# Optimization experiments

Hardware: AMD Instinct MI355X
Metric: run time of the kernel (lower is better)

## Reference

```python
import jax, jax.numpy as jnp
import numpy as np

N_NODES = 100000
N_EDGES = 3200000
D = 128


def setup_inputs() -> dict:
    key = jax.random.key(0)
    k1, k2, k3 = jax.random.split(key, 3)
    x = jax.random.normal(k1, (N_NODES, D), dtype=jnp.float32)
    edge_index = jax.random.randint(k2, (2, N_EDGES), 0, N_NODES, dtype=jnp.int64)
    W = jax.random.normal(k3, (D, D), dtype=jnp.float32) / np.sqrt(D)
    b = jnp.zeros((D,), dtype=jnp.float32)
    return {"x": x, "edge_index": edge_index, "W": W, "b": b}


def reference(x, edge_index, W, b):
    N = x.shape[0]
    # GCNConv: add self loops
    loop = jnp.arange(N, dtype=edge_index.dtype)
    src = jnp.concatenate([edge_index[0], loop])  # message source j
    dst = jnp.concatenate([edge_index[1], loop])  # aggregation target i
    # symmetric normalization: deg counted at targets (incl. self loops)
    deg = jax.ops.segment_sum(jnp.ones_like(dst, dtype=x.dtype), dst, num_segments=N)
    dinv = deg ** -0.5  # every node has deg >= 1 due to self loops
    norm = dinv[src] * dinv[dst]  # [E+N]
    # linear transform then gather-scale-scatter aggregation
    h = x @ W  # [N, D_out]
    msgs = h[src] * norm[:, None]  # [E+N, D_out]
    out = jax.ops.segment_sum(msgs, dst, num_segments=N) + b
    return jax.nn.relu(out)
```

## Files before the change

kernel.cpp:

```cpp
#include <hip/hip_runtime.h>

#define NN 100000
#define NE 3200000
#define DD 128
#define NB 391
#define NCH 256
#define CHUNK (NE / NCH)
#define PSTAGE 9216


typedef __attribute__((ext_vector_type(8))) short bf16x8;
typedef __attribute__((ext_vector_type(4))) float f32x4;

__device__ inline unsigned bf16pair(float a, float b) {
    unsigned ua = __float_as_uint(a); ua = (ua + 0x7fffu + ((ua >> 16) & 1u)) >> 16;
    unsigned ub = __float_as_uint(b); ub = (ub + 0x7fffu + ((ub >> 16) & 1u)) >> 16;
    return ua | (ub << 16);
}
__device__ inline float bflo(unsigned u) { return __uint_as_float(u << 16); }
__device__ inline float bfhi(unsigned u) { return __uint_as_float(u & 0xffff0000u); }

__global__ __launch_bounds__(256) void k_hist1(const int* __restrict__ dst, int* __restrict__ H,
                                               const float* __restrict__ W, unsigned* __restrict__ Wimg) {
    if (blockIdx.x < 32) {
        int i = blockIdx.x * 256 + threadIdx.x;
        int c = i >> 6, k2 = i & 63;
        unsigned v = bf16pair(W[(size_t)(k2 * 2) * DD + c], W[(size_t)(k2 * 2 + 1) * DD + c]);
        int byte = c * 256 + ((k2 * 4) ^ ((c & 7) << 4));
        *(unsigned*)((char*)Wimg + byte) = v;
    }
    __shared__ int h[NB];
    for (int i = threadIdx.x; i < NB; i += 256) h[i] = 0;
    __syncthreads();
    const int base = blockIdx.x * CHUNK;
    for (int i = threadIdx.x; i < CHUNK; i += 256)
        atomicAdd(&h[dst[base + i] >> 8], 1);
    __syncthreads();
    for (int i = threadIdx.x; i < NB; i += 256) H[blockIdx.x * NB + i] = h[i];
}

__global__ __launch_bounds__(256) void k_offB1(int* __restrict__ H, int* __restrict__ BT) {
    __shared__ int s[256];
    const int b = blockIdx.x;
    const int t = threadIdx.x;
    int v = H[t * NB + b];
    s[t] = v;
    __syncthreads();
    for (int off = 1; off < 256; off <<= 1) {
        int u = (t >= off) ? s[t - off] : 0;
        __syncthreads();
        s[t] += u;
        __syncthreads();
    }
    H[t * NB + b] = s[t] - v;
    if (t == 255) BT[b] = s[255];
}

__global__ __launch_bounds__(512) void k_offB2(const int* __restrict__ BT, int* __restrict__ BB) {
    __shared__ int s[512];
    const int t = threadIdx.x;
    int v = (t < NB) ? BT[t] : 0;
    s[t] = v;
    __syncthreads();
    for (int off = 1; off < 512; off <<= 1) {
        int u = (t >= off) ? s[t - off] : 0;
        __syncthreads();
        s[t] += u;
        __syncthreads();
    }
    if (t < NB) BB[t] = s[t] - v;
}

__global__ __launch_bounds__(256) void k_part(const int* __restrict__ src, const int* __restrict__ dst,
                                              const int* __restrict__ H, const int* __restrict__ BB,
                                              unsigned* __restrict__ P) {
    __shared__ int cur[NB];
    for (int i = threadIdx.x; i < NB; i += 256)
        cur[i] = BB[i] + H[blockIdx.x * NB + i];
    __syncthreads();
    const int base = blockIdx.x * CHUNK;
    for (int i = threadIdx.x; i < CHUNK; i += 256) {
        int s = src[base + i];
        int d = dst[base + i];
        int p = atomicAdd(&cur[d >> 8], 1);
        P[p] = ((unsigned)s << 8) | (unsigned)(d & 255);
    }
}

__global__ __launch_bounds__(256) void k_bsort(const unsigned* __restrict__ P, const int* __restrict__ BB,
                                               const int* __restrict__ BT, int* __restrict__ esrc,
                                               int* __restrict__ cnt, int* __restrict__ start) {
    __shared__ int hist[256], red[256], sexcl[256], fil[256];
    __shared__ unsigned Ps[PSTAGE];
    const int b = blockIdx.x;
    const int base = BB[b];
    const int n = BT[b];
    const int t = threadIdx.x;
    const bool fits = (n <= PSTAGE);
    hist[t] = 0;
    __syncthreads();
    for (int i = t; i < n; i += 256) {
        unsigned p = P[base + i];
        if (fits) Ps[i] = p;
        atomicAdd(&hist[p & 255u], 1);
    }
    __syncthreads();
    int c = hist[t];
    red[t] = c;
    __syncthreads();
    for (int off = 1; off < 256; off <<= 1) {
        int u = (t >= off) ? red[t - off] : 0;
        __syncthreads();
        red[t] += u;
        __syncthreads();
    }
    int excl = red[t] - c;
    sexcl[t] = excl;
    fil[t] = 0;
    int node = (b << 8) + t;
    if (node < NN) { cnt[node] = c; start[node] = base + excl; }
    __syncthreads();
    for (int i = t; i < n; i += 256) {
        unsigned p = fits ? Ps[i] : P[base + i];
        int dl = (int)(p & 255u);
        int pos = atomicAdd(&fil[dl], 1);
        esrc[base + sexcl[dl] + pos] = (int)(p >> 8);
    }
}

__global__ __launch_bounds__(256) void k_gemm_mfma(
    const float* __restrict__ x, const unsigned* __restrict__ Wimg,
    const int* __restrict__ cnt, unsigned* __restrict__ g) {
    __shared__ unsigned Wl[8192];
    const int tid = threadIdx.x;
    {
        const uint4* s4 = (const uint4*)Wimg;
        uint4* d4 = (uint4*)Wl;
        for (int i = tid; i < 2048; i += 256) d4[i] = s4[i];
    }
    const int row0 = blockIdx.x * 128;
    const int w = tid >> 6;
    const int l = tid & 63;
    const int lr = l & 15, lk = l >> 4;
    bf16x8 a[2][4];
#pragma unroll
    for (int rg = 0; rg < 2; ++rg) {
        int r = row0 + w * 32 + rg * 16 + lr;
        if (r > NN - 1) r = NN - 1;
        const float* xr = x + (size_t)r * DD;
#pragma unroll
        for (int kk = 0; kk < 4; ++kk) {
            float4 f0 = *(const float4*)(xr + kk * 32 + lk * 8);
            float4 f1 = *(const float4*)(xr + kk * 32 + lk * 8 + 4);
            uint4 wv;
            wv.x = bf16pair(f0.x, f0.y); wv.y = bf16pair(f0.z, f0.w);
            wv.z = bf16pair(f1.x, f1.y); wv.w = bf16pair(f1.z, f1.w);
            a[rg][kk] = *(bf16x8*)&wv;
        }
    }
    __syncthreads();
    f32x4 acc[2][8];
#pragma unroll
    for (int rg = 0; rg < 2; ++rg)
#pragma unroll
        for (int t = 0; t < 8; ++t) acc[rg][t] = (f32x4){0.f, 0.f, 0.f, 0.f};
#pragma unroll
    for (int t = 0; t < 8; ++t) {
        int c = t * 16 + lr;
#pragma unroll
        for (int kk = 0; kk < 4; ++kk) {
            int byte = c * 256 + ((kk * 64 + lk * 16) ^ ((c & 7) << 4));
            bf16x8 bfr = *(bf16x8*)((char*)Wl + byte);
            acc[0][t] = __builtin_amdgcn_mfma_f32_16x16x32_bf16(a[0][kk], bfr, acc[0][t], 0, 0, 0);
            acc[1][t] = __builtin_amdgcn_mfma_f32_16x16x32_bf16(a[1][kk], bfr, acc[1][t], 0, 0, 0);
        }
    }
#pragma unroll
    for (int rg = 0; rg < 2; ++rg)
#pragma unroll
    for (int j = 0; j < 4; ++j) {
        int row = row0 + w * 32 + rg * 16 + lk * 4 + j;
        if (row < NN) {
            float dinv = rsqrtf((float)(cnt[row] + 1));
#pragma unroll
            for (int t = 0; t < 4; ++t) {
                unsigned v = bf16pair(acc[rg][t][j] * dinv, acc[rg][t + 4][j] * dinv);
                g[(size_t)row * 64 + t * 16 + lr] = v;
            }
        }
    }
}

__global__ __launch_bounds__(256) void k_aggregate(
    const unsigned* __restrict__ g, const int* __restrict__ esrc,
    const int* __restrict__ start, const int* __restrict__ cnt,
    const float* __restrict__ b, float* __restrict__ out) {
    int node = blockIdx.x * 4 + (threadIdx.x >> 6);
    if (node >= NN) return;
    int lane = threadIdx.x & 63;
    unsigned u0 = g[(unsigned)node * 64u + lane];
    float ax = bflo(u0), ay = bfhi(u0);
    const int base = start[node];
    const int n = cnt[node];
    const int* ep = esrc + base;
    int j = 0;
    for (; j + 16 <= n; j += 16) {
        unsigned v[16];
#pragma unroll
        for (int u = 0; u < 16; ++u)
            v[u] = g[(unsigned)ep[j + u] * 64u + lane];
#pragma unroll
        for (int u = 0; u < 16; ++u) { ax += bflo(v[u]); ay += bfhi(v[u]); }
    }
    for (; j + 4 <= n; j += 4) {
        unsigned v0 = g[(unsigned)ep[j + 0] * 64u + lane];
        unsigned v1 = g[(unsigned)ep[j + 1] * 64u + lane];
        unsigned v2 = g[(unsigned)ep[j + 2] * 64u + lane];
        unsigned v3 = g[(unsigned)ep[j + 3] * 64u + lane];
        ax += bflo(v0) + bflo(v1) + bflo(v2) + bflo(v3);
        ay += bfhi(v0) + bfhi(v1) + bfhi(v2) + bfhi(v3);
    }
    for (; j < n; ++j) {
        unsigned v = g[(unsigned)ep[j] * 64u + lane];
        ax += bflo(v); ay += bfhi(v);
    }
    float dinv = rsqrtf((float)(n + 1));
    float bx = b[lane], by = b[lane + 64];
    float ox = fmaxf(fmaf(ax, dinv, bx), 0.f);
    float oy = fmaxf(fmaf(ay, dinv, by), 0.f);
    __builtin_nontemporal_store(ox, &out[(size_t)node * DD + lane]);
    __builtin_nontemporal_store(oy, &out[(size_t)node * DD + lane + 64]);
}

extern "C" void kernel_launch(void* const* d_in, const int* in_sizes, int n_in,
                              void* d_out, int out_size, void* d_ws, size_t ws_size,
                              hipStream_t stream) {
    const float* x = (const float*)d_in[0];
    const int* edge = (const int*)d_in[1];
    const float* W = (const float*)d_in[2];
    const float* b = (const float*)d_in[3];
    float* out = (float*)d_out;

    char* ws = (char*)d_ws;
    int* cnt      = (int*)(ws);
    int* start    = (int*)(ws + 400 * 1024);
    int* BT       = (int*)(ws + 800 * 1024);
    int* BB       = (int*)(ws + 804 * 1024);
    unsigned* Wim = (unsigned*)(ws + 832 * 1024);
    int* H        = (int*)(ws + (1 << 20));
    int* esrc     = (int*)(ws + (2 << 20));
    unsigned* P   = (unsigned*)(ws + (15ull << 20));
    unsigned* g   = (unsigned*)(ws + (15ull << 20));

    const int* src = edge;
    const int* dst = edge + NE;

    k_hist1<<<NCH, 256, 0, stream>>>(dst, H, W, Wim);
    k_offB1<<<NB, 256, 0, stream>>>(H, BT);
    k_offB2<<<1, 512, 0, stream>>>(BT, BB);
    k_part<<<NCH, 256, 0, stream>>>(src, dst, H, BB, P);
    k_bsort<<<NB, 256, 0, stream>>>(P, BB, BT, esrc, cnt, start);
    k_gemm_mfma<<<(NN + 127) / 128, 256, 0, stream>>>(x, Wim, cnt, g);
    k_aggregate<<<(NN + 3) / 4, 256, 0, stream>>>(g, esrc, start, cnt, b, out);
}
```

Before: 201.2 us.

## Slice gathered features into column slabs and drop the global bucket-offset scan kernel

The intermediate feature matrix is stored as 8 column slices of 32 bytes per node, so each aggregation block handles one slice and a wave gathers 8 neighbours at once. The aim is a smaller L2 working set per slice pass and better cache locality for random gathers. A partial-sum shuffle reduction combines the 8 slots. Separately, the single-block offB2 scan is replaced by an atomicAdd on a global cursor, which saves one launch. That makes bucket order nondeterministic, but each bucket's range stays contiguous. The catch is that each gather now moves only 32-byte segments and edge indices are reread 8 times.

```diff
diff --git a/kernel.cpp b/kernel.cpp
--- a/kernel.cpp
+++ b/kernel.cpp
@@ -7,6 +7,7 @@
 #define NCH 256
 #define CHUNK (NE / NCH)
 #define PSTAGE 9216
+#define SL (NN * 8)
 
 
 typedef __attribute__((ext_vector_type(8))) short bf16x8;
@@ -21,7 +22,9 @@
 __device__ inline float bfhi(unsigned u) { return __uint_as_float(u & 0xffff0000u); }
 
 __global__ __launch_bounds__(256) void k_hist1(const int* __restrict__ dst, int* __restrict__ H,
-                                               const float* __restrict__ W, unsigned* __restrict__ Wimg) {
+                                               const float* __restrict__ W, unsigned* __restrict__ Wimg,
+                                               int* __restrict__ gcur) {
+    if (blockIdx.x == 0 && threadIdx.x == 0) *gcur = 0;
     if (blockIdx.x < 32) {
         int i = blockIdx.x * 256 + threadIdx.x;
         int c = i >> 6, k2 = i & 63;
@@ -39,7 +42,8 @@
     for (int i = threadIdx.x; i < NB; i += 256) H[blockIdx.x * NB + i] = h[i];
 }
 
-__global__ __launch_bounds__(256) void k_offB1(int* __restrict__ H, int* __restrict__ BT) {
+__global__ __launch_bounds__(256) void k_offB1(int* __restrict__ H, int* __restrict__ BT,
+                                               int* __restrict__ BB, int* __restrict__ gcur) {
     __shared__ int s[256];
     const int b = blockIdx.x;
     const int t = threadIdx.x;
@@ -53,22 +57,10 @@
         __syncthreads();
     }
     H[t * NB + b] = s[t] - v;
-    if (t == 255) BT[b] = s[255];
-}
-
-__global__ __launch_bounds__(512) void k_offB2(const int* __restrict__ BT, int* __restrict__ BB) {
-    __shared__ int s[512];
-    const int t = threadIdx.x;
-    int v = (t < NB) ? BT[t] : 0;
-    s[t] = v;
-    __syncthreads();
-    for (int off = 1; off < 512; off <<= 1) {
-        int u = (t >= off) ? s[t - off] : 0;
-        __syncthreads();
-        s[t] += u;
-        __syncthreads();
-    }
-    if (t < NB) BB[t] = s[t] - v;
+    if (t == 255) {
+        BT[b] = s[255];
+        BB[b] = atomicAdd(gcur, s[255]);
+    }
 }
 
 __global__ __launch_bounds__(256) void k_part(const int* __restrict__ src, const int* __restrict__ dst,
@@ -130,7 +122,7 @@
 
 __global__ __launch_bounds__(256) void k_gemm_mfma(
     const float* __restrict__ x, const unsigned* __restrict__ Wimg,
-    const int* __restrict__ cnt, unsigned* __restrict__ g) {
+    const int* __restrict__ cnt, unsigned* __restrict__ g_s) {
     __shared__ unsigned Wl[8192];
     const int tid = threadIdx.x;
     {
@@ -184,52 +176,60 @@
             float dinv = rsqrtf((float)(cnt[row] + 1));
 #pragma unroll
             for (int t = 0; t < 4; ++t) {
+                int col = t * 16 + lr;
                 unsigned v = bf16pair(acc[rg][t][j] * dinv, acc[rg][t + 4][j] * dinv);
-                g[(size_t)row * 64 + t * 16 + lr] = v;
+                g_s[(size_t)(col >> 3) * SL + (size_t)row * 8 + (col & 7)] = v;
             }
         }
     }
 }
 
 __global__ __launch_bounds__(256) void k_aggregate(
-    const unsigned* __restrict__ g, const int* __restrict__ esrc,
+    const unsigned* __restrict__ g_s, const int* __restrict__ esrc,
     const int* __restrict__ start, const int* __restrict__ cnt,
     const float* __restrict__ b, float* __restrict__ out) {
-    int node = blockIdx.x * 4 + (threadIdx.x >> 6);
-    if (node >= NN) return;
-    int lane = threadIdx.x & 63;
-    unsigned u0 = g[(unsigned)node * 64u + lane];
-    float ax = bflo(u0), ay = bfhi(u0);
+    const int slice = blockIdx.x & 7;
+    const int node = (blockIdx.x >> 3) * 4 + (threadIdx.x >> 6);
+    const int lane = threadIdx.x & 63;
+    const int slot = lane >> 3;
+    const int c = lane & 7;
+    const unsigned* gs = g_s + (size_t)slice * SL + c;
+    float ax = 0.f, ay = 0.f;
+    if (slot == 0) {
+        unsigned v = gs[(unsigned)node * 8u];
+        ax = bflo(v); ay = bfhi(v);
+    }
     const int base = start[node];
     const int n = cnt[node];
     const int* ep = esrc + base;
     int j = 0;
-    for (; j + 16 <= n; j += 16) {
-        unsigned v[16];
-#pragma unroll
-        for (int u = 0; u < 16; ++u)
-            v[u] = g[(unsigned)ep[j + u] * 64u + lane];
-#pragma unroll
-        for (int u = 0; u < 16; ++u) { ax += bflo(v[u]); ay += bfhi(v[u]); }
-    }
-    for (; j + 4 <= n; j += 4) {
-        unsigned v0 = g[(unsigned)ep[j + 0] * 64u + lane];
-        unsigned v1 = g[(unsigned)ep[j + 1] * 64u + lane];
-        unsigned v2 = g[(unsigned)ep[j + 2] * 64u + lane];
-        unsigned v3 = g[(unsigned)ep[j + 3] * 64u + lane];
+    for (; j + 32 <= n; j += 32) {
+        unsigned v0 = gs[(unsigned)ep[j + slot] * 8u];
+        unsigned v1 = gs[(unsigned)ep[j + 8 + slot] * 8u];
+        unsigned v2 = gs[(unsigned)ep[j + 16 + slot] * 8u];
+        unsigned v3 = gs[(unsigned)ep[j + 24 + slot] * 8u];
         ax += bflo(v0) + bflo(v1) + bflo(v2) + bflo(v3);
         ay += bfhi(v0) + bfhi(v1) + bfhi(v2) + bfhi(v3);
     }
-    for (; j < n; ++j) {
-        unsigned v = g[(unsigned)ep[j] * 64u + lane];
+    for (; j + 8 <= n; j += 8) {
+        unsigned v = gs[(unsigned)ep[j + slot] * 8u];
         ax += bflo(v); ay += bfhi(v);
     }
-    float dinv = rsqrtf((float)(n + 1));
-    float bx = b[lane], by = b[lane + 64];
-    float ox = fmaxf(fmaf(ax, dinv, bx), 0.f);
-    float oy = fmaxf(fmaf(ay, dinv, by), 0.f);
-    __builtin_nontemporal_store(ox, &out[(size_t)node * DD + lane]);
-    __builtin_nontemporal_store(oy, &out[(size_t)node * DD + lane + 64]);
+    if (j < n && slot < n - j) {
+        unsigned v = gs[(unsigned)ep[j + slot] * 8u];
+        ax += bflo(v); ay += bfhi(v);
+    }
+    ax += __shfl_xor(ax, 8);  ay += __shfl_xor(ay, 8);
+    ax += __shfl_xor(ax, 16); ay += __shfl_xor(ay, 16);
+    ax += __shfl_xor(ax, 32); ay += __shfl_xor(ay, 32);
+    if (slot == 0) {
+        float dinv = rsqrtf((float)(n + 1));
+        int col = slice * 8 + c;
+        float ox = fmaxf(fmaf(ax, dinv, b[col]), 0.f);
+        float oy = fmaxf(fmaf(ay, dinv, b[col + 64]), 0.f);
+        __builtin_nontemporal_store(ox, &out[(size_t)node * DD + col]);
+        __builtin_nontemporal_store(oy, &out[(size_t)node * DD + col + 64]);
+    }
 }
 
 extern "C" void kernel_launch(void* const* d_in, const int* in_sizes, int n_in,
@@ -246,20 +246,20 @@
     int* start    = (int*)(ws + 400 * 1024);
     int* BT       = (int*)(ws + 800 * 1024);
     int* BB       = (int*)(ws + 804 * 1024);
+    int* gcur     = (int*)(ws + 808 * 1024);
     unsigned* Wim = (unsigned*)(ws + 832 * 1024);
     int* H        = (int*)(ws + (1 << 20));
     int* esrc     = (int*)(ws + (2 << 20));
     unsigned* P   = (unsigned*)(ws + (15ull << 20));
-    unsigned* g   = (unsigned*)(ws + (15ull << 20));
+    unsigned* g_s = (unsigned*)(ws + (15ull << 20));
 
     const int* src = edge;
     const int* dst = edge + NE;
 
-    k_hist1<<<NCH, 256, 0, stream>>>(dst, H, W, Wim);
-    k_offB1<<<NB, 256, 0, stream>>>(H, BT);
-    k_offB2<<<1, 512, 0, stream>>>(BT, BB);
+    k_hist1<<<NCH, 256, 0, stream>>>(dst, H, W, Wim, gcur);
+    k_offB1<<<NB, 256, 0, stream>>>(H, BT, BB, gcur);
     k_part<<<NCH, 256, 0, stream>>>(src, dst, H, BB, P);
     k_bsort<<<NB, 256, 0, stream>>>(P, BB, BT, esrc, cnt, start);
-    k_gemm_mfma<<<(NN + 127) / 128, 256, 0, stream>>>(x, Wim, cnt, g);
-    k_aggregate<<<(NN + 3) / 4, 256, 0, stream>>>(g, esrc, start, cnt, b, out);
-}
+    k_gemm_mfma<<<(NN + 127) / 128, 256, 0, stream>>>(x, Wim, cnt, g_s);
+    k_aggregate<<<(NN / 4) * 8, 256, 0, stream>>>(g_s, esrc, start, cnt, b, out);
+}
```

New measurement: 357.2 us. 77.6% more time.
